# Performance work log

Hardware: AMD Instinct MI355X
Metric: run time of the kernel (lower is better)

## Reference

```python
import math
import jax, jax.numpy as jnp
import numpy as np

N_HEADS = 16
D_EMBED = 1024
D_HEAD = D_EMBED // N_HEADS


def setup_inputs() -> dict:
    key = jax.random.key(0)
    k1, k2, k3, k4, k5 = jax.random.split(key, 5)
    B, S, D = 4, 2048, D_EMBED
    scale = 1.0 / math.sqrt(D)
    return {
        "x": jax.random.normal(k1, (B, S, D), dtype=jnp.float32),
        "in_proj_w": jax.random.normal(k2, (3 * D, D), dtype=jnp.float32) * scale,
        "in_proj_b": jax.random.normal(k3, (3 * D,), dtype=jnp.float32) * 0.02,
        "out_proj_w": jax.random.normal(k4, (D, D), dtype=jnp.float32) * scale,
        "out_proj_b": jax.random.normal(k5, (D,), dtype=jnp.float32) * 0.02,
        "causal_mask": 0,
    }


def reference(x, in_proj_w, in_proj_b, out_proj_w, out_proj_b, causal_mask):
    B, S, D = x.shape
    # in_proj: torch Linear -> x @ W^T + b, then chunk into q,k,v
    qkv = x @ in_proj_w.T + in_proj_b              # [B,S,3D]
    q, k, v = jnp.split(qkv, 3, axis=-1)
    # [B,S,D] -> [B,H,S,d]
    def heads(t):
        return t.reshape(B, S, N_HEADS, D_HEAD).transpose(0, 2, 1, 3)
    q, k, v = heads(q), heads(k), heads(v)
    weight = jnp.einsum("bhsd,bhtd->bhst", q, k)   # [B,H,S,S] materialized scores
    if causal_mask:
        mask = jnp.triu(jnp.ones((S, S), dtype=bool), k=1)
        weight = jnp.where(mask, -jnp.inf, weight)
    weight = jax.nn.softmax(weight / math.sqrt(D_HEAD), axis=-1)
    out = jnp.einsum("bhst,bhtd->bhsd", weight, v)  # [B,H,S,d]
    out = out.transpose(0, 2, 1, 3).reshape(B, S, D)
    return out @ out_proj_w.T + out_proj_b
```

## Files before the change

### kernel.cpp

```cpp
#include <hip/hip_runtime.h>

typedef unsigned short u16;
typedef _Float16 h8 __attribute__((ext_vector_type(8)));
typedef __fp16 fp16x2 __attribute__((ext_vector_type(2)));
typedef float f32x4 __attribute__((ext_vector_type(4)));

constexpr int B_ = 4, S_ = 2048, D_ = 1024, H_ = 16;

__device__ __forceinline__ void async16(const void* g, void* l) {
  __builtin_amdgcn_global_load_lds(
      (const __attribute__((address_space(1))) void*)g,
      (__attribute__((address_space(3))) void*)l, 16, 0, 0);
}

__device__ __forceinline__ unsigned pk2(float a, float b) {
  union { fp16x2 h; unsigned u; } c;
  c.h = __builtin_amdgcn_cvt_pkrtz(a, b);
  return c.u;
}

__global__ __launch_bounds__(256) void cvt_kernel(
    const float* __restrict__ src, _Float16* __restrict__ dst, int n)
{
  const int i = (blockIdx.x * 256 + threadIdx.x) * 4;
  if (i >= n) return;
  const float4 v = *(const float4*)(src + i);
  uint2 o;
  o.x = pk2(v.x, v.y);
  o.y = pk2(v.z, v.w);
  *(uint2*)(dst + i) = o;
}

template<bool OUT_HALF>
__global__ __launch_bounds__(256) void gemm_f16(
    const _Float16* __restrict__ A, const _Float16* __restrict__ Bw,
    const float* __restrict__ bias, void* __restrict__ Cout,
    int M, int N, int K)
{
  __shared__ __align__(16) _Float16 sA[2][4096];
  __shared__ __align__(16) _Float16 sB[2][4096];

  const int tid = threadIdx.x;
  const int lane = tid & 63, w = tid >> 6;
  const int wm = w & 1, wn = w >> 1;
  const int m0 = blockIdx.y * 128, n0 = blockIdx.x * 128;

  const int sr = 16 * w + (lane & 15);
  const int ss = lane >> 4;
  const _Float16* gA1 = A + (size_t)(m0 + sr) * K + 8 * ss;
  const _Float16* gA2 = gA1 + (size_t)64 * K;
  const _Float16* gB1 = Bw + (size_t)(n0 + sr) * K + 8 * ss;
  const _Float16* gB2 = gB1 + (size_t)64 * K;

  const f32x4 zf = {0.f, 0.f, 0.f, 0.f};
  f32x4 acc[4][4];
#pragma unroll
  for (int i = 0; i < 4; ++i)
#pragma unroll
    for (int j = 0; j < 4; ++j) acc[i][j] = zf;

  async16(gA1, &sA[0][w * 512]);
  async16(gA2, &sA[0][(w + 4) * 512]);
  async16(gB1, &sB[0][w * 512]);
  async16(gB2, &sB[0][(w + 4) * 512]);

  const int NIT = K >> 5;
  for (int it = 0; it < NIT; ++it) {
    const int cur = it & 1;
    __syncthreads();
    if (it + 1 < NIT) {
      const int kn = (it + 1) << 5;
      async16(gA1 + kn, &sA[cur ^ 1][w * 512]);
      async16(gA2 + kn, &sA[cur ^ 1][(w + 4) * 512]);
      async16(gB1 + kn, &sB[cur ^ 1][w * 512]);
      async16(gB2 + kn, &sB[cur ^ 1][(w + 4) * 512]);
    }

    h8 fa[4], fb[4];
#pragma unroll
    for (int i = 0; i < 4; ++i) {
      fa[i] = *(const h8*)&sA[cur][((wm * 4 + i) << 9) + (lane << 3)];
      fb[i] = *(const h8*)&sB[cur][((wn * 4 + i) << 9) + (lane << 3)];
    }
#pragma unroll
    for (int i = 0; i < 4; ++i)
#pragma unroll
      for (int j = 0; j < 4; ++j)
        acc[i][j] = __builtin_amdgcn_mfma_f32_16x16x32_f16(fa[i], fb[j], acc[i][j], 0, 0, 0);
  }

  const int g = lane >> 4, cc = lane & 15;
#pragma unroll
  for (int j = 0; j < 4; ++j) {
    const int col = n0 + (wn * 4 + j) * 16 + cc;
    const float bv = bias[col];
#pragma unroll
    for (int i = 0; i < 4; ++i) {
      const int rowb = m0 + (wm * 4 + i) * 16 + g * 4;
#pragma unroll
      for (int r = 0; r < 4; ++r) {
        const float v = acc[i][j][r] + bv;
        if constexpr (OUT_HALF)
          ((_Float16*)Cout)[(size_t)(rowb + r) * N + col] = (_Float16)v;
        else
          ((float*)Cout)[(size_t)(rowb + r) * N + col] = v;
      }
    }
  }
}

__global__ __launch_bounds__(256) void transpose_v(
    const u16* __restrict__ qkv, u16* __restrict__ vT)
{
  __shared__ u16 T[64 * 73];
  const int tid = threadIdx.x;
  const int bh = blockIdx.y, s0 = blockIdx.x * 64;
  const int b = bh >> 4, h = bh & 15;
#pragma unroll
  for (int t = 0; t < 2; ++t) {
    const int c = tid + t * 256, r = c >> 3, cs = c & 7;
    union { int4 v; u16 s[8]; } u;
    u.v = *(const int4*)(qkv + (size_t)(b * S_ + s0 + r) * 3072 + 2048 + h * 64 + 8 * cs);
#pragma unroll
    for (int i = 0; i < 8; ++i) T[r * 73 + 8 * cs + i] = u.s[i];
  }
  __syncthreads();
#pragma unroll
  for (int t = 0; t < 2; ++t) {
    const int c = tid + t * 256, rd = c >> 3, ss = c & 7;
    union { int4 v; u16 s[8]; } u;
#pragma unroll
    for (int i = 0; i < 8; ++i) u.s[i] = T[(8 * ss + i) * 73 + rd];
    *(int4*)(vT + (size_t)(bh * 64 + rd) * S_ + s0 + 8 * ss) = u.v;
  }
}

__global__ __launch_bounds__(256, 4) void attn_f16(
    const _Float16* __restrict__ qkv, const _Float16* __restrict__ vT,
    _Float16* __restrict__ attnO, const int* __restrict__ causal_ptr)
{
  __shared__ __align__(16) _Float16 sQP[9216];
  __shared__ __align__(16) _Float16 sK[2][4096];
  __shared__ __align__(16) _Float16 sV[2][4096];

  const int tid = threadIdx.x, lane = tid & 63, w = tid >> 6;
  const int q4 = lane >> 4, cc = lane & 15;
  const int bh = blockIdx.y, b = bh >> 4, h = bh & 15;
  const int q0 = blockIdx.x * 128;
  const int causal = causal_ptr[0];

  {
    const int rr = lane & 15, sc8 = lane >> 4;
#pragma unroll
    for (int tt = 0; tt < 2; ++tt) {
      const int t = 2 * w + tt;
#pragma unroll
      for (int sh = 0; sh < 2; ++sh) {
        const _Float16* g = qkv + (size_t)(b * S_ + q0 + 16 * t + rr) * 3072 + h * 64 + 8 * (4 * sh + sc8);
        async16(g, &sQP[t * 1024 + sh * 512]);
      }
    }
  }

  const _Float16* gK = qkv + (size_t)(b * S_ + 16 * w + (lane & 15)) * 3072 + 1024 + h * 64 + 8 * (lane >> 4);
  const _Float16* gV = vT + (size_t)(bh * 64 + 16 * w + (lane & 15)) * S_ + 8 * (lane >> 4);

  async16(gK, &sK[0][w * 1024]);
  async16(gK + 32, &sK[0][w * 1024 + 512]);
  async16(gV, &sV[0][w * 1024]);
  async16(gV + 32, &sV[0][w * 1024 + 512]);

  __syncthreads();

  h8 qf[2][2];
#pragma unroll
  for (int m = 0; m < 2; ++m)
#pragma unroll
    for (int kk = 0; kk < 2; ++kk) {
      h8 v = *(const h8*)&sQP[((2 * w + m) << 10) + (kk << 9) + (lane << 3)];
      qf[m][kk] = v * (_Float16)0.125f;
    }

  h8 ones;
#pragma unroll
  for (int i = 0; i < 8; ++i) ones[i] = (_Float16)1.0f;

  const int wp = w * 2304;

  const f32x4 zf = {0.f, 0.f, 0.f, 0.f};
  f32x4 oa[2][4], lac[2];
#pragma unroll
  for (int m = 0; m < 2; ++m) {
    lac[m] = zf;
#pragma unroll
    for (int nt = 0; nt < 4; ++nt) oa[m][nt] = zf;
  }

  const int nit = causal ? (q0 / 64 + 2) : (S_ / 64);

  for (int it = 0; it < nit; ++it) {
    const int cur = it & 1;
    const int j0 = it * 64;
    __syncthreads();
    if (it + 1 < nit) {
      const size_t jn = (size_t)(j0 + 64);
      async16(gK + jn * 3072, &sK[cur ^ 1][w * 1024]);
      async16(gK + jn * 3072 + 32, &sK[cur ^ 1][w * 1024 + 512]);
      async16(gV + jn, &sV[cur ^ 1][w * 1024]);
      async16(gV + jn + 32, &sV[cur ^ 1][w * 1024 + 512]);
    }

    f32x4 sc[2][4];
#pragma unroll
    for (int nt = 0; nt < 4; ++nt) {
      const h8 kf0 = *(const h8*)&sK[cur][(nt << 10) + (lane << 3)];
      const h8 kf1 = *(const h8*)&sK[cur][(nt << 10) + 512 + (lane << 3)];
#pragma unroll
      for (int m = 0; m < 2; ++m) {
        sc[m][nt] = __builtin_amdgcn_mfma_f32_16x16x32_f16(kf0, qf[m][0], zf, 0, 0, 0);
        sc[m][nt] = __builtin_amdgcn_mfma_f32_16x16x32_f16(kf1, qf[m][1], sc[m][nt], 0, 0, 0);
      }
    }

    if (causal) {
#pragma unroll
      for (int m = 0; m < 2; ++m)
#pragma unroll
        for (int nt = 0; nt < 4; ++nt)
#pragma unroll
          for (int r = 0; r < 4; ++r)
            if ((j0 + nt * 16 + q4 * 4 + r) > (q0 + 32 * w + m * 16 + cc))
              sc[m][nt][r] = -1.0e30f;
    }

#pragma unroll
    for (int m = 0; m < 2; ++m)
#pragma unroll
      for (int nt = 0; nt < 4; ++nt) {
        uint2 pk;
        pk.x = pk2(__expf(sc[m][nt][0]), __expf(sc[m][nt][1]));
        pk.y = pk2(__expf(sc[m][nt][2]), __expf(sc[m][nt][3]));
        *(uint2*)&sQP[wp + (m * 16 + cc) * 72 + nt * 16 + q4 * 4] = pk;
      }

    asm volatile("s_waitcnt lgkmcnt(0)" ::: "memory");

    h8 pf[2][2];
#pragma unroll
    for (int m = 0; m < 2; ++m)
#pragma unroll
      for (int kk = 0; kk < 2; ++kk)
        pf[m][kk] = *(const h8*)&sQP[wp + (m * 16 + cc) * 72 + kk * 32 + q4 * 8];

#pragma unroll
    for (int m = 0; m < 2; ++m) {
      lac[m] = __builtin_amdgcn_mfma_f32_16x16x32_f16(pf[m][0], ones, lac[m], 0, 0, 0);
      lac[m] = __builtin_amdgcn_mfma_f32_16x16x32_f16(pf[m][1], ones, lac[m], 0, 0, 0);
    }
#pragma unroll
    for (int nt = 0; nt < 4; ++nt) {
      const h8 vf0 = *(const h8*)&sV[cur][(nt << 10) + (lane << 3)];
      const h8 vf1 = *(const h8*)&sV[cur][(nt << 10) + 512 + (lane << 3)];
#pragma unroll
      for (int m = 0; m < 2; ++m) {
        oa[m][nt] = __builtin_amdgcn_mfma_f32_16x16x32_f16(pf[m][0], vf0, oa[m][nt], 0, 0, 0);
        oa[m][nt] = __builtin_amdgcn_mfma_f32_16x16x32_f16(pf[m][1], vf1, oa[m][nt], 0, 0, 0);
      }
    }
  }

#pragma unroll
  for (int m = 0; m < 2; ++m) {
    float inv[4];
#pragma unroll
    for (int r = 0; r < 4; ++r) inv[r] = 1.0f / lac[m][r];
#pragma unroll
    for (int nt = 0; nt < 4; ++nt) {
      const int col = h * 64 + nt * 16 + cc;
#pragma unroll
      for (int r = 0; r < 4; ++r) {
        const int row = b * S_ + q0 + 32 * w + m * 16 + q4 * 4 + r;
        attnO[(size_t)row * D_ + col] = (_Float16)(oa[m][nt][r] * inv[r]);
      }
    }
  }
}

extern "C" void kernel_launch(void* const* d_in, const int* in_sizes, int n_in,
                              void* d_out, int out_size, void* d_ws, size_t ws_size,
                              hipStream_t stream)
{
  const float* x  = (const float*)d_in[0];
  const float* wi = (const float*)d_in[1];
  const float* bi = (const float*)d_in[2];
  const float* wo = (const float*)d_in[3];
  const float* bo = (const float*)d_in[4];
  const int* causal = (const int*)d_in[5];

  _Float16* xh   = (_Float16*)d_ws;
  _Float16* wih  = xh + 8388608;
  _Float16* woh  = wih + 3145728;
  _Float16* qkvb = woh + 1048576;
  _Float16* vT   = qkvb + 25165824;
  _Float16* attn = vT + 8388608;

  const int M = B_ * S_;

  cvt_kernel<<<8192, 256, 0, stream>>>(x, xh, M * D_);
  cvt_kernel<<<3072, 256, 0, stream>>>(wi, wih, 3 * D_ * D_);
  cvt_kernel<<<1024, 256, 0, stream>>>(wo, woh, D_ * D_);

  gemm_f16<true><<<dim3(24, 64), 256, 0, stream>>>(
      xh, wih, bi, qkvb, M, 3 * D_, D_);

  transpose_v<<<dim3(32, 64), 256, 0, stream>>>((const u16*)qkvb, (u16*)vT);

  attn_f16<<<dim3(16, 64), 256, 0, stream>>>(qkvb, vT, attn, causal);

  gemm_f16<false><<<dim3(8, 64), 256, 0, stream>>>(
      attn, woh, bo, d_out, M, D_, D_);
}
```

Baseline: 363.1 us.

## Use wider 128x256 GEMM tile for QKV projection, single-buffer attention K/V, exp2 softmax

Adds a gemm_wide kernel with 128x256 tiles and 4x8 MFMA accumulators per wave for the QKV projection, raising arithmetic intensity and halving the block count. The attention kernel drops K/V double-buffering in favour of a synchronous load with two barriers per iteration. This reduces LDS use but removes load/compute overlap. Softmax now uses exp2f with log2(e) folded into the Q scale factor, making each exponential cheaper.

New measurement: 351.3 us. -3.2%, faster.

```diff
diff --git a/kernel.cpp b/kernel.cpp
--- a/kernel.cpp
+++ b/kernel.cpp
@@ -29,6 +29,86 @@
   o.x = pk2(v.x, v.y);
   o.y = pk2(v.z, v.w);
   *(uint2*)(dst + i) = o;
+}
+
+template<bool OUT_HALF>
+__global__ __launch_bounds__(256, 2) void gemm_wide(
+    const _Float16* __restrict__ A, const _Float16* __restrict__ Bw,
+    const float* __restrict__ bias, void* __restrict__ Cout,
+    int M, int N, int K)
+{
+  __shared__ __align__(16) _Float16 sA[2][4096];
+  __shared__ __align__(16) _Float16 sB[2][8192];
+
+  const int tid = threadIdx.x;
+  const int lane = tid & 63, w = tid >> 6;
+  const int wm = w & 1, wn = w >> 1;
+  const int m0 = blockIdx.y * 128, n0 = blockIdx.x * 256;
+
+  const int sr = 16 * w + (lane & 15);
+  const int ss = lane >> 4;
+  const _Float16* gA1 = A + (size_t)(m0 + sr) * K + 8 * ss;
+  const _Float16* gA2 = gA1 + (size_t)64 * K;
+  const _Float16* gB1 = Bw + (size_t)(n0 + sr) * K + 8 * ss;
+
+  const f32x4 zf = {0.f, 0.f, 0.f, 0.f};
+  f32x4 acc[4][8];
+#pragma unroll
+  for (int i = 0; i < 4; ++i)
+#pragma unroll
+    for (int j = 0; j < 8; ++j) acc[i][j] = zf;
+
+  async16(gA1, &sA[0][w * 512]);
+  async16(gA2, &sA[0][(w + 4) * 512]);
+#pragma unroll
+  for (int t = 0; t < 4; ++t)
+    async16(gB1 + (size_t)(64 * t) * K, &sB[0][(w + 4 * t) * 512]);
+
+  const int NIT = K >> 5;
+  for (int it = 0; it < NIT; ++it) {
+    const int cur = it & 1;
+    __syncthreads();
+    if (it + 1 < NIT) {
+      const int kn = (it + 1) << 5;
+      async16(gA1 + kn, &sA[cur ^ 1][w * 512]);
+      async16(gA2 + kn, &sA[cur ^ 1][(w + 4) * 512]);
+#pragma unroll
+      for (int t = 0; t < 4; ++t)
+        async16(gB1 + (size_t)(64 * t) * K + kn, &sB[cur ^ 1][(w + 4 * t) * 512]);
+    }
+
+    h8 fa[4], fb[8];
+#pragma unroll
+    for (int i = 0; i < 4; ++i)
+      fa[i] = *(const h8*)&sA[cur][((wm * 4 + i) << 9) + (lane << 3)];
+#pragma unroll
+    for (int j = 0; j < 8; ++j)
+      fb[j] = *(const h8*)&sB[cur][((wn * 8 + j) << 9) + (lane << 3)];
+#pragma unroll
+    for (int i = 0; i < 4; ++i)
+#pragma unroll
+      for (int j = 0; j < 8; ++j)
+        acc[i][j] = __builtin_amdgcn_mfma_f32_16x16x32_f16(fa[i], fb[j], acc[i][j], 0, 0, 0);
+  }
+
+  const int g = lane >> 4, cc = lane & 15;
+#pragma unroll
+  for (int j = 0; j < 8; ++j) {
+    const int col = n0 + (wn * 8 + j) * 16 + cc;
+    const float bv = bias[col];
+#pragma unroll
+    for (int i = 0; i < 4; ++i) {
+      const int rowb = m0 + (wm * 4 + i) * 16 + g * 4;
+#pragma unroll
+      for (int r = 0; r < 4; ++r) {
+        const float v = acc[i][j][r] + bv;
+        if constexpr (OUT_HALF)
+          ((_Float16*)Cout)[(size_t)(rowb + r) * N + col] = (_Float16)v;
+        else
+          ((float*)Cout)[(size_t)(rowb + r) * N + col] = v;
+      }
+    }
+  }
 }
 
 template<bool OUT_HALF>
@@ -140,8 +220,8 @@
     _Float16* __restrict__ attnO, const int* __restrict__ causal_ptr)
 {
   __shared__ __align__(16) _Float16 sQP[9216];
-  __shared__ __align__(16) _Float16 sK[2][4096];
-  __shared__ __align__(16) _Float16 sV[2][4096];
+  __shared__ __align__(16) _Float16 sK[4096];
+  __shared__ __align__(16) _Float16 sV[4096];
 
   const int tid = threadIdx.x, lane = tid & 63, w = tid >> 6;
   const int q4 = lane >> 4, cc = lane & 15;
@@ -161,29 +241,25 @@
       }
     }
   }
+  __syncthreads();
+
+  h8 qf[2][2];
+#pragma unroll
+  for (int m = 0; m < 2; ++m)
+#pragma unroll
+    for (int kk = 0; kk < 2; ++kk) {
+      h8 v = *(const h8*)&sQP[((2 * w + m) << 10) + (kk << 9) + (lane << 3)];
+      qf[m][kk] = v * (_Float16)0.18033688f;
+    }
+
+  h8 ones;
+#pragma unroll
+  for (int i = 0; i < 8; ++i) ones[i] = (_Float16)1.0f;
 
   const _Float16* gK = qkv + (size_t)(b * S_ + 16 * w + (lane & 15)) * 3072 + 1024 + h * 64 + 8 * (lane >> 4);
   const _Float16* gV = vT + (size_t)(bh * 64 + 16 * w + (lane & 15)) * S_ + 8 * (lane >> 4);
-
-  async16(gK, &sK[0][w * 1024]);
-  async16(gK + 32, &sK[0][w * 1024 + 512]);
-  async16(gV, &sV[0][w * 1024]);
-  async16(gV + 32, &sV[0][w * 1024 + 512]);
-
-  __syncthreads();
-
-  h8 qf[2][2];
-#pragma unroll
-  for (int m = 0; m < 2; ++m)
-#pragma unroll
-    for (int kk = 0; kk < 2; ++kk) {
-      h8 v = *(const h8*)&sQP[((2 * w + m) << 10) + (kk << 9) + (lane << 3)];
-      qf[m][kk] = v * (_Float16)0.125f;
-    }
-
-  h8 ones;
-#pragma unroll
-  for (int i = 0; i < 8; ++i) ones[i] = (_Float16)1.0f;
+  _Float16* lK0 = &sK[w * 1024];
+  _Float16* lV0 = &sV[w * 1024];
 
   const int wp = w * 2304;
 
@@ -199,22 +275,19 @@
   const int nit = causal ? (q0 / 64 + 2) : (S_ / 64);
 
   for (int it = 0; it < nit; ++it) {
-    const int cur = it & 1;
     const int j0 = it * 64;
     __syncthreads();
-    if (it + 1 < nit) {
-      const size_t jn = (size_t)(j0 + 64);
-      async16(gK + jn * 3072, &sK[cur ^ 1][w * 1024]);
-      async16(gK + jn * 3072 + 32, &sK[cur ^ 1][w * 1024 + 512]);
-      async16(gV + jn, &sV[cur ^ 1][w * 1024]);
-      async16(gV + jn + 32, &sV[cur ^ 1][w * 1024 + 512]);
-    }
+    async16(gK + (size_t)j0 * 3072, lK0);
+    async16(gK + (size_t)j0 * 3072 + 32, lK0 + 512);
+    async16(gV + j0, lV0);
+    async16(gV + j0 + 32, lV0 + 512);
+    __syncthreads();
 
     f32x4 sc[2][4];
 #pragma unroll
     for (int nt = 0; nt < 4; ++nt) {
-      const h8 kf0 = *(const h8*)&sK[cur][(nt << 10) + (lane << 3)];
-      const h8 kf1 = *(const h8*)&sK[cur][(nt << 10) + 512 + (lane << 3)];
+      const h8 kf0 = *(const h8*)&sK[(nt << 10) + (lane << 3)];
+      const h8 kf1 = *(const h8*)&sK[(nt << 10) + 512 + (lane << 3)];
 #pragma unroll
       for (int m = 0; m < 2; ++m) {
         sc[m][nt] = __builtin_amdgcn_mfma_f32_16x16x32_f16(kf0, qf[m][0], zf, 0, 0, 0);
@@ -238,8 +311,8 @@
 #pragma unroll
       for (int nt = 0; nt < 4; ++nt) {
         uint2 pk;
-        pk.x = pk2(__expf(sc[m][nt][0]), __expf(sc[m][nt][1]));
-        pk.y = pk2(__expf(sc[m][nt][2]), __expf(sc[m][nt][3]));
+        pk.x = pk2(exp2f(sc[m][nt][0]), exp2f(sc[m][nt][1]));
+        pk.y = pk2(exp2f(sc[m][nt][2]), exp2f(sc[m][nt][3]));
         *(uint2*)&sQP[wp + (m * 16 + cc) * 72 + nt * 16 + q4 * 4] = pk;
       }
 
@@ -259,8 +332,8 @@
     }
 #pragma unroll
     for (int nt = 0; nt < 4; ++nt) {
-      const h8 vf0 = *(const h8*)&sV[cur][(nt << 10) + (lane << 3)];
-      const h8 vf1 = *(const h8*)&sV[cur][(nt << 10) + 512 + (lane << 3)];
+      const h8 vf0 = *(const h8*)&sV[(nt << 10) + (lane << 3)];
+      const h8 vf1 = *(const h8*)&sV[(nt << 10) + 512 + (lane << 3)];
 #pragma unroll
       for (int m = 0; m < 2; ++m) {
         oa[m][nt] = __builtin_amdgcn_mfma_f32_16x16x32_f16(pf[m][0], vf0, oa[m][nt], 0, 0, 0);
@@ -310,7 +383,7 @@
   cvt_kernel<<<3072, 256, 0, stream>>>(wi, wih, 3 * D_ * D_);
   cvt_kernel<<<1024, 256, 0, stream>>>(wo, woh, D_ * D_);
 
-  gemm_f16<true><<<dim3(24, 64), 256, 0, stream>>>(
+  gemm_wide<true><<<dim3(12, 64), 256, 0, stream>>>(
       xh, wih, bi, qkvb, M, 3 * D_, D_);
 
   transpose_v<<<dim3(32, 64), 256, 0, stream>>>((const u16*)qkvb, (u16*)vT);
```
